# Kernel tuning notes

Hardware: AMD Instinct MI355X
Metric: run time of the kernel (lower is better)

## Reference

```python
import jax, jax.numpy as jnp
import numpy as np

B, L, D, H = 4, 8192, 1024, 8
Dh = D // H
EPS = 1e-4
PAD = 1  # circular padding on each side, kernel_size=3, stride=1


def setup_inputs() -> dict:
    key = jax.random.key(0)
    k1, k2, k3, k4, k5 = jax.random.split(key, 5)
    return {
        "x": jax.random.normal(k1, (B, L, D), dtype=jnp.float32),
        "hash_w": jax.random.normal(k2, (H, Dh, 2), dtype=jnp.float32) * 0.05,
        "hash_b": jax.random.normal(k3, (H, 2), dtype=jnp.float32) * 0.05,
        "conv_w": jax.random.normal(k4, (D, D // H, 3), dtype=jnp.float32) * 0.05,
        "conv_b": jax.random.normal(k5, (D,), dtype=jnp.float32) * 0.05,
    }


def reference(x, hash_w, hash_b, conv_w, conv_b):
    # x: [B, L, D]
    xh = x.reshape(B, L, H, Dh)
    # per-head 2-dim hash projection, concatenated as [x0,y0,x1,y1,...] on last dim
    proj = jnp.einsum('blhd,hdk->blhk', xh, hash_w) + hash_b  # [B,L,H,2]
    proj = proj.reshape(B, L, 2 * H)
    # faithful to torch.split(projected, n_heads, dim=2): first H vs last H channels
    h_x, h_y = proj[..., :H], proj[..., H:]
    angles = jnp.arctan(h_x / (h_y + EPS))  # [B,L,H]
    idx = jnp.argsort(angles, axis=1)       # [B,L,H] permutation along L per (b,h)
    # gather: reorder tokens per head
    xs = jnp.take_along_axis(xh, idx[..., None], axis=1)  # [B,L,H,Dh]
    # grouped circular Conv1d over the sorted sequence
    xc = xs.reshape(B, L, D).swapaxes(1, 2)               # [B,D,L]
    xc = jnp.pad(xc, ((0, 0), (0, 0), (PAD, PAD)), mode='wrap')
    y = jax.lax.conv_general_dilated(
        xc, conv_w, window_strides=(1,), padding='VALID',
        dimension_numbers=('NCH', 'OIH', 'NCH'), feature_group_count=H)
    y = y + conv_b[None, :, None]                          # [B,D,L]
    y = y.swapaxes(1, 2).reshape(B, L, H, Dh)
    # scatter back to original token order == gather with inverse permutation
    inv = jnp.argsort(idx, axis=1)
    out = jnp.take_along_axis(y, inv[..., None], axis=1)
    return out.reshape(B, L, D)
```

## Files before the change

kernel.cpp:

```cpp
#include <hip/hip_runtime.h>
#include <math.h>

#define LL 8192
#define DD 1024
#define DH 128

typedef unsigned long long u64;
typedef __attribute__((ext_vector_type(8))) short bf16x8;
typedef __attribute__((ext_vector_type(4))) float f32x4;

__device__ __forceinline__ unsigned short f2bf(float f) {
  unsigned u = __float_as_uint(f);
  u = (u + 0x7fffu + ((u >> 16) & 1u)) >> 16;
  return (unsigned short)u;
}

__device__ __forceinline__ float fdlibm_atanf(float x) {
#pragma clang fp contract(off)
  const float atanhi0 = __uint_as_float(0x3eed6338u);
  const float atanhi1 = __uint_as_float(0x3f490fdau);
  const float atanhi2 = __uint_as_float(0x3f7b985eu);
  const float atanhi3 = __uint_as_float(0x3fc90fdau);
  const float atanlo0 = __uint_as_float(0x31ac3769u);
  const float atanlo1 = __uint_as_float(0x33222168u);
  const float atanlo2 = __uint_as_float(0x33140fb4u);
  const float atanlo3 = __uint_as_float(0x33a22168u);
  const float aT0 = __uint_as_float(0x3eaaaaa9u);
  const float aT1 = __uint_as_float(0xbe4cca98u);
  const float aT2 = __uint_as_float(0x3e11f50du);
  const float aT3 = __uint_as_float(0xbdda1247u);
  const float aT4 = __uint_as_float(0x3d7cac25u);
  unsigned hx = __float_as_uint(x);
  unsigned ix = hx & 0x7fffffffu;
  int id;
  if (ix >= 0x4c800000u) {
    if (ix > 0x7f800000u) return x + x;
    float z = atanhi3 + atanlo3;
    return (hx >> 31) ? -z : z;
  }
  if (ix < 0x3ee00000u) {
    if (ix < 0x39800000u) return x;
    id = -1;
  } else {
    x = fabsf(x);
    if (ix < 0x3f980000u) {
      if (ix < 0x3f300000u) { id = 0; x = (2.0f * x - 1.0f) / (2.0f + x); }
      else                  { id = 1; x = (x - 1.0f) / (x + 1.0f); }
    } else {
      if (ix < 0x401c0000u) { id = 2; x = (x - 1.5f) / (1.0f + 1.5f * x); }
      else                  { id = 3; x = -1.0f / x; }
    }
  }
  float z = x * x;
  float w = z * z;
  float s1 = z * (aT0 + w * (aT2 + w * aT4));
  float s2 = w * (aT1 + w * aT3);
  if (id < 0) return x - x * (s1 + s2);
  float r;
  if (id == 0)      r = atanhi0 - ((x * (s1 + s2) - atanlo0) - x);
  else if (id == 1) r = atanhi1 - ((x * (s1 + s2) - atanlo1) - x);
  else if (id == 2) r = atanhi2 - ((x * (s1 + s2) - atanlo2) - x);
  else              r = atanhi3 - ((x * (s1 + s2) - atanlo3) - x);
  return (hx >> 31) ? -r : r;
}

__global__ __launch_bounds__(256) void k_keys(const float* __restrict__ x,
                                              const float* __restrict__ hw,
                                              const float* __restrict__ hb,
                                              u64* __restrict__ ks,
                                              const float* __restrict__ cw,
                                              unsigned short* __restrict__ wb) {
  __shared__ float2 wL[128][8];
  __shared__ float projL[32][16];
  const int tid = threadIdx.x;
  const float2* hw2 = (const float2*)hw;
  for (int i = tid; i < 1024; i += 256) {
    int hh = i >> 7, dd = i & 127;
    wL[dd][hh] = hw2[i];
  }
  __syncthreads();
  const int r = tid >> 3;
  const int h = tid & 7;
  const int m = blockIdx.x * 32 + r;
  const float4* xp = (const float4*)(x + (size_t)m * DD + h * DH);
  float a0 = 0.f, a1 = 0.f;
#pragma unroll
  for (int q = 0; q < 32; ++q) {
    float4 v = xp[q];
    float2 w0 = wL[q * 4 + 0][h];
    float2 w1 = wL[q * 4 + 1][h];
    float2 w2 = wL[q * 4 + 2][h];
    float2 w3 = wL[q * 4 + 3][h];
    a0 = fmaf(v.x, w0.x, a0); a1 = fmaf(v.x, w0.y, a1);
    a0 = fmaf(v.y, w1.x, a0); a1 = fmaf(v.y, w1.y, a1);
    a0 = fmaf(v.z, w2.x, a0); a1 = fmaf(v.z, w2.y, a1);
    a0 = fmaf(v.w, w3.x, a0); a1 = fmaf(v.w, w3.y, a1);
  }
  projL[r][h * 2 + 0] = a0;
  projL[r][h * 2 + 1] = a1;
  __syncthreads();
  const int j = h;
  float px = projL[r][j] + hb[j];
  float py = projL[r][8 + j] + hb[8 + j];
  float den = py + 1e-4f;
  float ratio = px / den;
  float angle = fdlibm_atanf(ratio);
  unsigned am = __float_as_uint(angle);
  am = (am & 0x80000000u) ? ~am : (am | 0x80000000u);
  const int b = m >> 13, l = m & (LL - 1);
  ks[((size_t)b * 8 + j) * LL + l] = ((u64)am << 13) | (u64)l;
  {
    int base = blockIdx.x * 384;
    for (int g = base + tid; g < base + 384; g += 256) {
      int hh = g / 49152;
      int rem = g % 49152;
      int kk = rem >> 12;
      int rem2 = rem & 4095;
      int n = rem2 >> 9;
      int rem3 = rem2 & 511;
      int l2 = rem3 >> 3;
      int j2 = rem3 & 7;
      int k = kk * 32 + ((l2 >> 4) * 8) + j2;
      int o = n * 16 + (l2 & 15);
      int t = k >> 7, i2 = k & 127;
      wb[g] = f2bf(cw[((size_t)(hh * 128 + o)) * 384 + i2 * 3 + t]);
    }
  }
}

__global__ __launch_bounds__(256) void k_sort_loc512(u64* __restrict__ ks) {
  __shared__ u64 sk[512];
  const int blk = blockIdx.x;
  const int seg = blk >> 4, c = blk & 15;
  u64* base = ks + (size_t)seg * LL + c * 512;
  const int tid = threadIdx.x;
  sk[tid] = base[tid];
  sk[tid + 256] = base[tid + 256];
  __syncthreads();
  const int cb = c * 512;
  for (int size = 2; size <= 512; size <<= 1) {
    for (int stride = size >> 1; stride > 0; stride >>= 1) {
      int i = 2 * tid - (tid & (stride - 1));
      int j = i + stride;
      bool up = (((cb + i) & size) == 0);
      u64 a = sk[i], d = sk[j];
      if ((a > d) == up) { sk[i] = d; sk[j] = a; }
      __syncthreads();
    }
  }
  base[tid] = sk[tid];
  base[tid + 256] = sk[tid + 256];
}

__global__ __launch_bounds__(1024) void k_sort_loc2k(u64* __restrict__ ks) {
  __shared__ u64 sk[2048];
  const int blk = blockIdx.x;
  const int seg = blk >> 2, c = blk & 3;
  u64* base = ks + (size_t)seg * LL + c * 2048;
  const int tid = threadIdx.x;
  sk[tid] = base[tid];
  sk[tid + 1024] = base[tid + 1024];
  __syncthreads();
  const int cb = c * 2048;
  for (int size = 1024; size <= 2048; size <<= 1) {
    for (int stride = size >> 1; stride > 0; stride >>= 1) {
      int i = 2 * tid - (tid & (stride - 1));
      int j = i + stride;
      bool up = (((cb + i) & size) == 0);
      u64 a = sk[i], d = sk[j];
      if ((a > d) == up) { sk[i] = d; sk[j] = a; }
      __syncthreads();
    }
  }
  base[tid] = sk[tid];
  base[tid + 1024] = sk[tid + 1024];
}

__global__ __launch_bounds__(1024) void k_sort_t4k(u64* __restrict__ ks) {
  __shared__ u64 sk[4096];
  const int blk = blockIdx.x;
  const int seg = blk >> 1, c = blk & 1;
  u64* base = ks + (size_t)seg * LL + c * 4096;
  const int tid = threadIdx.x;
#pragma unroll
  for (int i = 0; i < 4; ++i) sk[tid + i * 1024] = base[tid + i * 1024];
  __syncthreads();
  const int cb = c * 4096;
  for (int stride = 2048; stride > 0; stride >>= 1) {
#pragma unroll
    for (int pp = 0; pp < 2; ++pp) {
      int p = tid + pp * 1024;
      int i = 2 * p - (p & (stride - 1));
      int j = i + stride;
      bool up = (((cb + i) & 4096) == 0);
      u64 a = sk[i], d = sk[j];
      if ((a > d) == up) { sk[i] = d; sk[j] = a; }
    }
    __syncthreads();
  }
#pragma unroll
  for (int i = 0; i < 4; ++i) base[tid + i * 1024] = sk[tid + i * 1024];
}

__global__ __launch_bounds__(256) void k_sort_g8(u64* __restrict__ ks) {
  int t = blockIdx.x * 256 + threadIdx.x;
  int seg = t >> 11, i = t & 2047;
  u64* base = ks + (size_t)seg * LL;
  u64 e0 = base[i], e1 = base[i + 2048], e2 = base[i + 4096], e3 = base[i + 6144];
  u64 tt;
  if (e0 > e2) { tt = e0; e0 = e2; e2 = tt; }
  if (e1 > e3) { tt = e1; e1 = e3; e3 = tt; }
  if (e0 > e1) { tt = e0; e0 = e1; e1 = tt; }
  if (e2 > e3) { tt = e2; e2 = e3; e3 = tt; }
  base[i] = e0; base[i + 2048] = e1; base[i + 4096] = e2; base[i + 6144] = e3;
}

__global__ __launch_bounds__(1024) void k_sort_tail(u64* __restrict__ ks,
                                                    int size,
                                                    int* __restrict__ perm) {
  __shared__ u64 sk[2048];
  const int blk = blockIdx.x;
  const int seg = blk >> 2, c = blk & 3;
  u64* base = ks + (size_t)seg * LL + c * 2048;
  const int tid = threadIdx.x;
  sk[tid] = base[tid];
  sk[tid + 1024] = base[tid + 1024];
  __syncthreads();
  const int cb = c * 2048;
  for (int stride = 1024; stride > 0; stride >>= 1) {
    int i = 2 * tid - (tid & (stride - 1));
    int j = i + stride;
    bool up = (((cb + i) & size) == 0);
    u64 a = sk[i], d = sk[j];
    if ((a > d) == up) { sk[i] = d; sk[j] = a; }
    __syncthreads();
  }
  if (perm) {
    int* dst = perm + (size_t)seg * LL + c * 2048;
    dst[tid] = (int)(sk[tid] & (u64)(LL - 1));
    dst[tid + 1024] = (int)(sk[tid + 1024] & (u64)(LL - 1));
  } else {
    base[tid] = sk[tid];
    base[tid + 1024] = sk[tid + 1024];
  }
}

__global__ __launch_bounds__(256) void k_conv(const float* __restrict__ x,
                                              const unsigned short* __restrict__ wb,
                                              const float* __restrict__ bias,
                                              const int* __restrict__ perm,
                                              float* __restrict__ out) {
  __shared__ short Xs[66 * 136];
  __shared__ int Ps[64];
  const int tid = threadIdx.x;
  const int bid = blockIdx.x;
  const int tile = bid & 127;
  const int h = (bid >> 7) & 7;
  const int b = bid >> 10;
  const int r0 = tile * 64;
  const int* pbh = perm + ((size_t)b * 8 + h) * LL;
  if (tid < 64) Ps[tid] = pbh[r0 + tid];
  {
    const int ln = tid & 31;
    for (int j = (tid >> 5); j < 66; j += 8) {
      int rank = (r0 + j - 1 + LL) & (LL - 1);
      int src = pbh[rank];
      float4 v = ((const float4*)(x + ((size_t)(b * LL + src)) * DD + h * DH))[ln];
      uint2 pk;
      pk.x = (unsigned)f2bf(v.x) | ((unsigned)f2bf(v.y) << 16);
      pk.y = (unsigned)f2bf(v.z) | ((unsigned)f2bf(v.w) << 16);
      *(uint2*)(Xs + j * 136 + ln * 4) = pk;
    }
  }
  const int w = tid >> 6;
  const int l = tid & 63;
  const int arow = w * 16 + (l & 15);
  const int acol = (l >> 4) * 8;
  f32x4 acc[8];
#pragma unroll
  for (int n = 0; n < 8; ++n) acc[n] = (f32x4){0.f, 0.f, 0.f, 0.f};
  const bf16x8* wfrag = (const bf16x8*)(wb + (size_t)h * 49152 + (size_t)l * 8);
  __syncthreads();
  for (int kk = 0; kk < 12; ++kk) {
    bf16x8 af = *(const bf16x8*)(Xs + (arow + (kk >> 2)) * 136 + (kk & 3) * 32 + acol);
#pragma unroll
    for (int n = 0; n < 8; ++n) {
      bf16x8 bfr = wfrag[(kk * 8 + n) * 64];
      acc[n] = __builtin_amdgcn_mfma_f32_16x16x32_bf16(af, bfr, acc[n], 0, 0, 0);
    }
  }
  int dsts[4];
#pragma unroll
  for (int reg = 0; reg < 4; ++reg) dsts[reg] = Ps[w * 16 + (l >> 4) * 4 + reg];
#pragma unroll
  for (int n = 0; n < 8; ++n) {
    int o = h * DH + n * 16 + (l & 15);
    float bv = bias[o];
#pragma unroll
    for (int reg = 0; reg < 4; ++reg) {
      out[((size_t)(b * LL + dsts[reg])) * DD + o] = acc[n][reg] + bv;
    }
  }
}

extern "C" void kernel_launch(void* const* d_in, const int* in_sizes, int n_in,
                              void* d_out, int out_size, void* d_ws, size_t ws_size,
                              hipStream_t stream) {
  const float* x  = (const float*)d_in[0];
  const float* hw = (const float*)d_in[1];
  const float* hb = (const float*)d_in[2];
  const float* cw = (const float*)d_in[3];
  const float* cb = (const float*)d_in[4];
  float* out = (float*)d_out;
  u64* ks   = (u64*)d_ws;
  int* perm = (int*)((char*)d_ws + (2u << 20));
  unsigned short* wbp = (unsigned short*)((char*)d_ws + (3u << 20));

  k_keys<<<1024, 256, 0, stream>>>(x, hw, hb, ks, cw, wbp);
  k_sort_loc512<<<512, 256, 0, stream>>>(ks);
  k_sort_loc2k<<<128, 1024, 0, stream>>>(ks);
  k_sort_t4k<<<64, 1024, 0, stream>>>(ks);
  k_sort_g8<<<256, 256, 0, stream>>>(ks);
  k_sort_tail<<<128, 1024, 0, stream>>>(ks, 8192, perm);
  k_conv<<<4096, 256, 0, stream>>>(x, wbp, cb, perm, out);
}
```

Measured before the change: 136.1 us.

## Swap MFMA operand roles so each lane writes contiguous float4 outputs

After: 130.6 us. 4.1% less time.

```diff
diff --git a/kernel.cpp b/kernel.cpp
--- a/kernel.cpp
+++ b/kernel.cpp
@@ -274,31 +274,39 @@
   }
   const int w = tid >> 6;
   const int l = tid & 63;
-  const int arow = w * 16 + (l & 15);
-  const int acol = (l >> 4) * 8;
-  f32x4 acc[8];
-#pragma unroll
-  for (int n = 0; n < 8; ++n) acc[n] = (f32x4){0.f, 0.f, 0.f, 0.f};
-  const bf16x8* wfrag = (const bf16x8*)(wb + (size_t)h * 49152 + (size_t)l * 8);
+  const int q = l >> 4;
+  const int r16 = l & 15;
+  f32x4 acc[2][4];
+#pragma unroll
+  for (int ot = 0; ot < 2; ++ot)
+#pragma unroll
+    for (int rt = 0; rt < 4; ++rt) acc[ot][rt] = (f32x4){0.f, 0.f, 0.f, 0.f};
+  const bf16x8* wf = (const bf16x8*)(wb + (size_t)h * 49152 + (size_t)l * 8);
   __syncthreads();
   for (int kk = 0; kk < 12; ++kk) {
-    bf16x8 af = *(const bf16x8*)(Xs + (arow + (kk >> 2)) * 136 + (kk & 3) * 32 + acol);
-#pragma unroll
-    for (int n = 0; n < 8; ++n) {
-      bf16x8 bfr = wfrag[(kk * 8 + n) * 64];
-      acc[n] = __builtin_amdgcn_mfma_f32_16x16x32_bf16(af, bfr, acc[n], 0, 0, 0);
-    }
-  }
-  int dsts[4];
-#pragma unroll
-  for (int reg = 0; reg < 4; ++reg) dsts[reg] = Ps[w * 16 + (l >> 4) * 4 + reg];
-#pragma unroll
-  for (int n = 0; n < 8; ++n) {
-    int o = h * DH + n * 16 + (l & 15);
-    float bv = bias[o];
-#pragma unroll
-    for (int reg = 0; reg < 4; ++reg) {
-      out[((size_t)(b * LL + dsts[reg])) * DD + o] = acc[n][reg] + bv;
+    bf16x8 wa0 = wf[(kk * 8 + w * 2 + 0) * 64];
+    bf16x8 wa1 = wf[(kk * 8 + w * 2 + 1) * 64];
+    const short* xbase = Xs + (kk >> 2) * 136 + (kk & 3) * 32 + q * 8;
+#pragma unroll
+    for (int rt = 0; rt < 4; ++rt) {
+      bf16x8 xb = *(const bf16x8*)(xbase + (rt * 16 + r16) * 136);
+      acc[0][rt] = __builtin_amdgcn_mfma_f32_16x16x32_bf16(wa0, xb, acc[0][rt], 0, 0, 0);
+      acc[1][rt] = __builtin_amdgcn_mfma_f32_16x16x32_bf16(wa1, xb, acc[1][rt], 0, 0, 0);
+    }
+  }
+  const int obase = h * DH + w * 32;
+#pragma unroll
+  for (int ot = 0; ot < 2; ++ot) {
+    float4 bv = *(const float4*)(bias + obase + ot * 16 + q * 4);
+#pragma unroll
+    for (int rt = 0; rt < 4; ++rt) {
+      int dst = Ps[rt * 16 + r16];
+      float4 v;
+      v.x = acc[ot][rt][0] + bv.x;
+      v.y = acc[ot][rt][1] + bv.y;
+      v.z = acc[ot][rt][2] + bv.z;
+      v.w = acc[ot][rt][3] + bv.w;
+      *(float4*)(out + ((size_t)(b * LL + dst)) * DD + obase + ot * 16 + q * 4) = v;
     }
   }
 }
```
